# Kernel optimization log

Measured on AMD Instinct MI355X. Metric: run time of the kernel, lower is better.

Reference implementation:

```python
import jax, jax.numpy as jnp
import numpy as np

TOP_K = 2


def setup_inputs() -> dict:
    key = jax.random.key(0)
    k1, k2 = jax.random.split(key)
    x = jax.random.normal(k1, (4, 4096, 2048), dtype=jnp.float32)
    W = jax.random.normal(k2, (64, 2048), dtype=jnp.float32) * (1.0 / np.sqrt(2048))
    return {"x": x, "W": W}


def reference(x, W):
    B, S, D = x.shape
    E = W.shape[0]
    # logits: [B*S, E] via linear router (no bias)
    flat = x.reshape(-1, D)
    logits = jnp.einsum('td,ed->te', flat, W)
    probs = jax.nn.softmax(logits, axis=-1)
    # eval path: top-k indices
    _, top_k_indices = jax.lax.top_k(probs, TOP_K)          # [T, K]
    # scatter 1s -> mask; scatter gathered probs -> router_probs (== probs*mask)
    router_mask = jax.nn.one_hot(top_k_indices, E, dtype=probs.dtype).sum(axis=-2)  # [T, E]
    router_probs = probs * router_mask
    # normalize (top_k > 1: gradient flows through the sum)
    router_probs = router_probs / router_probs.sum(axis=-1, keepdims=True)
    return (router_mask.reshape(B, S, E),
            top_k_indices.reshape(B, S, TOP_K),
            router_probs.reshape(B, S, E),
            probs.reshape(B, S, E))
```

## Files before the change

### kernel.cpp

```cpp
#include <hip/hip_runtime.h>
#include <math.h>


#define D_DIM 2048
#define E_DIM 64

typedef __bf16 bf16x8 __attribute__((ext_vector_type(8)));
typedef unsigned short us8 __attribute__((ext_vector_type(8)));
typedef float f32x4 __attribute__((ext_vector_type(4)));

static __device__ __forceinline__ unsigned short f2bf(float f) {
    unsigned int u = __float_as_uint(f);
    u += 0x7fffu + ((u >> 16) & 1u);
    return (unsigned short)(u >> 16);
}
static __device__ __forceinline__ float bf2f(unsigned short h) {
    return __uint_as_float(((unsigned int)h) << 16);
}
static __device__ __forceinline__ void split4(const float4 v, ushort4* h, ushort4* l) {
    h->x = f2bf(v.x); l->x = f2bf(v.x - bf2f(h->x));
    h->y = f2bf(v.y); l->y = f2bf(v.y - bf2f(h->y));
    h->z = f2bf(v.z); l->z = f2bf(v.z - bf2f(h->z));
    h->w = f2bf(v.w); l->w = f2bf(v.w - bf2f(h->w));
}

static __device__ __forceinline__ void gld_lds16(const void* g, void* l) {
    __builtin_amdgcn_global_load_lds(
        (const __attribute__((address_space(1))) unsigned int*)g,
        (__attribute__((address_space(3))) unsigned int*)l,
        16, 0, 0);
}

__global__ __launch_bounds__(256, 1) void convert_w(
    const float4* __restrict__ W4, unsigned short* __restrict__ WH,
    unsigned short* __restrict__ WL)
{
    int i = blockIdx.x * 256 + threadIdx.x;
    float4 v = W4[i];
    ushort4 h, l;
    split4(v, &h, &l);
    *(ushort4*)&WH[i * 4] = h;
    *(ushort4*)&WL[i * 4] = l;
}

__global__ __launch_bounds__(256, 4) void router_fused(
    const float* __restrict__ x,
    const unsigned short* __restrict__ WHg, const unsigned short* __restrict__ WLg,
    float* __restrict__ mask_out, float* __restrict__ idx_out,
    float* __restrict__ rp_out, float* __restrict__ probs_out)
{
    __shared__ __align__(16) float          XF [2][16 * 64];
    __shared__ __align__(16) unsigned short WHs[2][64 * 64];
    __shared__ __align__(16) unsigned short WLs[2][64 * 64];

    const int tid  = threadIdx.x;
    const int lane = tid & 63;
    const int wv   = tid >> 6;
    const int quad = lane >> 4;
    const int l16  = lane & 15;

    const int t0  = blockIdx.x << 4;
    const int NCH = D_DIM >> 6;

    f32x4 acc = {0.f, 0.f, 0.f, 0.f};

    const int xrow = tid >> 4;
    const int xcg  = (tid & 15) ^ (xrow & 15);
    const int we   = wv * 8 + (lane >> 3);
    const int wo   = lane & 7;

    {
        gld_lds16(x + (size_t)(t0 + xrow) * D_DIM + xcg * 4,
                  &XF[0][(wv * 64) * 4]);
        #pragma unroll
        for (int i2 = 0; i2 < 2; ++i2) {
            int e  = i2 * 32 + we;
            int og = wo ^ (e & 7);
            gld_lds16(WHg + (size_t)e * D_DIM + og * 8,
                      &WHs[0][(i2 * 256 + wv * 64) * 8]);
            gld_lds16(WLg + (size_t)e * D_DIM + og * 8,
                      &WLs[0][(i2 * 256 + wv * 64) * 8]);
        }
    }
    __syncthreads();

    int buf = 0;
    for (int ch = 0; ch < NCH; ++ch) {
        if (ch + 1 < NCH) {
            const int kc = (ch + 1) << 6;
            const int nb = buf ^ 1;
            gld_lds16(x + (size_t)(t0 + xrow) * D_DIM + kc + xcg * 4,
                      &XF[nb][(wv * 64) * 4]);
            #pragma unroll
            for (int i2 = 0; i2 < 2; ++i2) {
                int e  = i2 * 32 + we;
                int og = wo ^ (e & 7);
                gld_lds16(WHg + (size_t)e * D_DIM + kc + og * 8,
                          &WHs[nb][(i2 * 256 + wv * 64) * 8]);
                gld_lds16(WLg + (size_t)e * D_DIM + kc + og * 8,
                          &WLs[nb][(i2 * 256 + wv * 64) * 8]);
            }
        }

        #pragma unroll
        for (int ks = 0; ks < 2; ++ks) {
            const int tr = l16;
            const int c0 = ks * 8 + quad * 2;
            float4 xa = *(const float4*)&XF[buf][(tr * 16 + ( c0      ^ (tr & 15))) * 4];
            float4 xb = *(const float4*)&XF[buf][(tr * 16 + ((c0 + 1) ^ (tr & 15))) * 4];
            ushort4 h0, l0, h1, l1;
            split4(xa, &h0, &l0);
            split4(xb, &h1, &l1);
            union { us8 u; bf16x8 b; } ua, ul;
            ua.u = (us8){h0.x, h0.y, h0.z, h0.w, h1.x, h1.y, h1.z, h1.w};
            ul.u = (us8){l0.x, l0.y, l0.z, l0.w, l1.x, l1.y, l1.z, l1.w};

            const int e = wv * 16 + l16;
            const int o = ks * 4 + quad;
            const int s = e * 8 + (o ^ (e & 7));
            bf16x8 bh = *(const bf16x8*)&WHs[buf][s * 8];
            bf16x8 bl = *(const bf16x8*)&WLs[buf][s * 8];
            acc = __builtin_amdgcn_mfma_f32_16x16x32_bf16(ua.b, bh, acc, 0, 0, 0);
            acc = __builtin_amdgcn_mfma_f32_16x16x32_bf16(ul.b, bh, acc, 0, 0, 0);
            acc = __builtin_amdgcn_mfma_f32_16x16x32_bf16(ua.b, bl, acc, 0, 0, 0);
        }
        __syncthreads();
        buf ^= 1;
    }

    float* L = &XF[0][0];
    #pragma unroll
    for (int r = 0; r < 4; ++r)
        L[(quad * 4 + r) * 64 + wv * 16 + l16] = acc[r];
    __syncthreads();

    for (int i = 0; i < 4; ++i) {
        const int tl = wv * 4 + i;
        const int t  = t0 + tl;
        const float v = L[tl * 64 + lane];

        float bv = v; int bi = lane;
        #pragma unroll
        for (int off = 1; off < 64; off <<= 1) {
            float ov = __shfl_xor(bv, off, 64);
            int   oi = __shfl_xor(bi, off, 64);
            bool take = (ov > bv) || (ov == bv && oi < bi);
            bv = take ? ov : bv;
            bi = take ? oi : bi;
        }
        const float m = bv; const int i1 = bi;

        const float p = __expf(v - m);
        float s = p;
        #pragma unroll
        for (int off = 1; off < 64; off <<= 1) s += __shfl_xor(s, off, 64);
        const float prob = p / s;

        const float v2 = (lane == i1) ? -INFINITY : v;
        float cv = v2; int ci = lane;
        #pragma unroll
        for (int off = 1; off < 64; off <<= 1) {
            float ov = __shfl_xor(cv, off, 64);
            int   oi = __shfl_xor(ci, off, 64);
            bool take = (ov > cv) || (ov == cv && oi < ci);
            cv = take ? ov : cv;
            ci = take ? oi : ci;
        }
        const int i2 = ci;

        const float pd = __shfl(prob, i1, 64) + __shfl(prob, i2, 64);
        const bool top = (lane == i1) || (lane == i2);

        const size_t base = (size_t)t * 64 + lane;
        mask_out[base]  = top ? 1.f : 0.f;
        rp_out[base]    = top ? prob / pd : 0.f;
        probs_out[base] = prob;
        if (lane == 0) {
            idx_out[(size_t)t * 2]     = (float)i1;
            idx_out[(size_t)t * 2 + 1] = (float)i2;
        }
    }
}

extern "C" void kernel_launch(void* const* d_in, const int* in_sizes, int n_in,
                              void* d_out, int out_size, void* d_ws, size_t ws_size,
                              hipStream_t stream) {
    const float* x = (const float*)d_in[0];
    const float* W = (const float*)d_in[1];
    float* out = (float*)d_out;

    const int T  = in_sizes[0] / D_DIM;
    const int WN = in_sizes[1];

    unsigned short* WH = (unsigned short*)d_ws;
    unsigned short* WL = WH + WN;

    float* mask_out  = out;
    float* idx_out   = out + (size_t)T * E_DIM;
    float* rp_out    = idx_out + (size_t)T * 2;
    float* probs_out = rp_out + (size_t)T * E_DIM;

    convert_w<<<dim3(WN / 1024), dim3(256), 0, stream>>>((const float4*)W, WH, WL);
    router_fused<<<dim3(T / 16), dim3(256), 0, stream>>>(
        x, WH, WL, mask_out, idx_out, rp_out, probs_out);
}
```

Baseline: 221.3 us.

## Split x into bf16 hi/lo once per element via register prefetch

```diff
diff --git a/kernel.cpp b/kernel.cpp
--- a/kernel.cpp
+++ b/kernel.cpp
@@ -4,6 +4,7 @@
 
 #define D_DIM 2048
 #define E_DIM 64
+#define NCH   (D_DIM >> 6)
 
 typedef __bf16 bf16x8 __attribute__((ext_vector_type(8)));
 typedef unsigned short us8 __attribute__((ext_vector_type(8)));
@@ -49,7 +50,8 @@
     float* __restrict__ mask_out, float* __restrict__ idx_out,
     float* __restrict__ rp_out, float* __restrict__ probs_out)
 {
-    __shared__ __align__(16) float          XF [2][16 * 64];
+    __shared__ __align__(16) unsigned short XH [2][16 * 64];
+    __shared__ __align__(16) unsigned short XL [2][16 * 64];
     __shared__ __align__(16) unsigned short WHs[2][64 * 64];
     __shared__ __align__(16) unsigned short WLs[2][64 * 64];
 
@@ -59,38 +61,50 @@
     const int quad = lane >> 4;
     const int l16  = lane & 15;
 
-    const int t0  = blockIdx.x << 4;
-    const int NCH = D_DIM >> 6;
+    const int t0 = blockIdx.x << 4;
 
     f32x4 acc = {0.f, 0.f, 0.f, 0.f};
 
-    const int xrow = tid >> 4;
-    const int xcg  = (tid & 15) ^ (xrow & 15);
-    const int we   = wv * 8 + (lane >> 3);
-    const int wo   = lane & 7;
-
-    {
-        gld_lds16(x + (size_t)(t0 + xrow) * D_DIM + xcg * 4,
-                  &XF[0][(wv * 64) * 4]);
-        #pragma unroll
-        for (int i2 = 0; i2 < 2; ++i2) {
-            int e  = i2 * 32 + we;
-            int og = wo ^ (e & 7);
-            gld_lds16(WHg + (size_t)e * D_DIM + og * 8,
-                      &WHs[0][(i2 * 256 + wv * 64) * 8]);
-            gld_lds16(WLg + (size_t)e * D_DIM + og * 8,
-                      &WLs[0][(i2 * 256 + wv * 64) * 8]);
-        }
+    const int we = wv * 8 + (lane >> 3);
+    const int wo = lane & 7;
+
+    const float* xg = x + (size_t)(t0 + l16) * D_DIM + wv * 16 + quad * 4;
+
+    const int g   = wv * 4 + quad;
+    const int cwb = l16 * 128 + (((g >> 1) ^ (l16 & 7)) << 4) + (g & 1) * 8;
+
+    float4 xc = *(const float4*)(xg);
+    #pragma unroll
+    for (int i2 = 0; i2 < 2; ++i2) {
+        int e  = i2 * 32 + we;
+        int og = wo ^ (e & 7);
+        gld_lds16(WHg + (size_t)e * D_DIM + og * 8, &WHs[0][(i2 * 256 + wv * 64) * 8]);
+        gld_lds16(WLg + (size_t)e * D_DIM + og * 8, &WLs[0][(i2 * 256 + wv * 64) * 8]);
     }
-    __syncthreads();
-
-    int buf = 0;
+
     for (int ch = 0; ch < NCH; ++ch) {
+        const int b = ch & 1;
+
+        float4 xn;
+        if (ch + 1 < NCH) xn = *(const float4*)(xg + (ch + 1) * 64);
+
+        {
+            ushort4 h, l;
+            split4(xc, &h, &l);
+            *(ushort4*)((char*)&XH[b][0] + cwb) = h;
+            *(ushort4*)((char*)&XL[b][0] + cwb) = l;
+        }
+
+        if (ch + 1 < NCH) asm volatile("s_waitcnt vmcnt(1)" ::: "memory");
+        else              asm volatile("s_waitcnt vmcnt(0)" ::: "memory");
+        asm volatile("s_waitcnt lgkmcnt(0)" ::: "memory");
+        __builtin_amdgcn_sched_barrier(0);
+        __builtin_amdgcn_s_barrier();
+        __builtin_amdgcn_sched_barrier(0);
+
         if (ch + 1 < NCH) {
             const int kc = (ch + 1) << 6;
-            const int nb = buf ^ 1;
-            gld_lds16(x + (size_t)(t0 + xrow) * D_DIM + kc + xcg * 4,
-                      &XF[nb][(wv * 64) * 4]);
+            const int nb = b ^ 1;
             #pragma unroll
             for (int i2 = 0; i2 < 2; ++i2) {
                 int e  = i2 * 32 + we;
@@ -104,31 +118,25 @@
 
         #pragma unroll
         for (int ks = 0; ks < 2; ++ks) {
-            const int tr = l16;
-            const int c0 = ks * 8 + quad * 2;
-            float4 xa = *(const float4*)&XF[buf][(tr * 16 + ( c0      ^ (tr & 15))) * 4];
-            float4 xb = *(const float4*)&XF[buf][(tr * 16 + ((c0 + 1) ^ (tr & 15))) * 4];
-            ushort4 h0, l0, h1, l1;
-            split4(xa, &h0, &l0);
-            split4(xb, &h1, &l1);
-            union { us8 u; bf16x8 b; } ua, ul;
-            ua.u = (us8){h0.x, h0.y, h0.z, h0.w, h1.x, h1.y, h1.z, h1.w};
-            ul.u = (us8){l0.x, l0.y, l0.z, l0.w, l1.x, l1.y, l1.z, l1.w};
+            const int sr = ks * 4 + quad;
+            const int ab = l16 * 128 + ((sr ^ (l16 & 7)) << 4);
+            bf16x8 ah = *(const bf16x8*)((const char*)&XH[b][0] + ab);
+            bf16x8 al = *(const bf16x8*)((const char*)&XL[b][0] + ab);
 
             const int e = wv * 16 + l16;
             const int o = ks * 4 + quad;
             const int s = e * 8 + (o ^ (e & 7));
-            bf16x8 bh = *(const bf16x8*)&WHs[buf][s * 8];
-            bf16x8 bl = *(const bf16x8*)&WLs[buf][s * 8];
-            acc = __builtin_amdgcn_mfma_f32_16x16x32_bf16(ua.b, bh, acc, 0, 0, 0);
-            acc = __builtin_amdgcn_mfma_f32_16x16x32_bf16(ul.b, bh, acc, 0, 0, 0);
-            acc = __builtin_amdgcn_mfma_f32_16x16x32_bf16(ua.b, bl, acc, 0, 0, 0);
-        }
-        __syncthreads();
-        buf ^= 1;
+            bf16x8 bh = *(const bf16x8*)&WHs[b][s * 8];
+            bf16x8 bl = *(const bf16x8*)&WLs[b][s * 8];
+            acc = __builtin_amdgcn_mfma_f32_16x16x32_bf16(ah, bh, acc, 0, 0, 0);
+            acc = __builtin_amdgcn_mfma_f32_16x16x32_bf16(al, bh, acc, 0, 0, 0);
+            acc = __builtin_amdgcn_mfma_f32_16x16x32_bf16(ah, bl, acc, 0, 0, 0);
+        }
+
+        if (ch + 1 < NCH) xc = xn;
     }
 
-    float* L = &XF[0][0];
+    float* L = (float*)&WHs[0][0];
     #pragma unroll
     for (int r = 0; r < 4; ++r)
         L[(quad * 4 + r) * 64 + wv * 16 + l16] = acc[r];
```

Result: no change. 218.3 us (-1.3%).

## Split K across waves with direct global loads instead of LDS double buffering

Applied to the files above, without the earlier changes.

```diff
diff --git a/kernel.cpp b/kernel.cpp
--- a/kernel.cpp
+++ b/kernel.cpp
@@ -24,13 +24,6 @@
     h->w = f2bf(v.w); l->w = f2bf(v.w - bf2f(h->w));
 }
 
-static __device__ __forceinline__ void gld_lds16(const void* g, void* l) {
-    __builtin_amdgcn_global_load_lds(
-        (const __attribute__((address_space(1))) unsigned int*)g,
-        (__attribute__((address_space(3))) unsigned int*)l,
-        16, 0, 0);
-}
-
 __global__ __launch_bounds__(256, 1) void convert_w(
     const float4* __restrict__ W4, unsigned short* __restrict__ WH,
     unsigned short* __restrict__ WL)
@@ -49,95 +42,59 @@
     float* __restrict__ mask_out, float* __restrict__ idx_out,
     float* __restrict__ rp_out, float* __restrict__ probs_out)
 {
-    __shared__ __align__(16) float          XF [2][16 * 64];
-    __shared__ __align__(16) unsigned short WHs[2][64 * 64];
-    __shared__ __align__(16) unsigned short WLs[2][64 * 64];
+    __shared__ __align__(16) float Lp[4][16 * 64];
 
     const int tid  = threadIdx.x;
     const int lane = tid & 63;
     const int wv   = tid >> 6;
     const int quad = lane >> 4;
     const int l16  = lane & 15;
+    const int t0   = blockIdx.x << 4;
 
-    const int t0  = blockIdx.x << 4;
-    const int NCH = D_DIM >> 6;
+    const int k0 = wv << 9;
 
-    f32x4 acc = {0.f, 0.f, 0.f, 0.f};
+    const float*          xp  = x   + (size_t)(t0 + l16) * D_DIM + k0 + quad * 8;
+    const unsigned short* whp = WHg + (size_t)l16 * D_DIM + k0 + quad * 8;
+    const unsigned short* wlp = WLg + (size_t)l16 * D_DIM + k0 + quad * 8;
 
-    const int xrow = tid >> 4;
-    const int xcg  = (tid & 15) ^ (xrow & 15);
-    const int we   = wv * 8 + (lane >> 3);
-    const int wo   = lane & 7;
+    f32x4 acc[4];
+    #pragma unroll
+    for (int n = 0; n < 4; ++n) { f32x4 z = {0.f, 0.f, 0.f, 0.f}; acc[n] = z; }
 
-    {
-        gld_lds16(x + (size_t)(t0 + xrow) * D_DIM + xcg * 4,
-                  &XF[0][(wv * 64) * 4]);
+    #pragma unroll 2
+    for (int j = 0; j < 16; ++j) {
+        const int o = j << 5;
+        float4 xa = *(const float4*)(xp + o);
+        float4 xb = *(const float4*)(xp + o + 4);
+        ushort4 h0, l0, h1, l1;
+        split4(xa, &h0, &l0);
+        split4(xb, &h1, &l1);
+        union { us8 u; bf16x8 b; } ua, ul;
+        ua.u = (us8){h0.x, h0.y, h0.z, h0.w, h1.x, h1.y, h1.z, h1.w};
+        ul.u = (us8){l0.x, l0.y, l0.z, l0.w, l1.x, l1.y, l1.z, l1.w};
+
         #pragma unroll
-        for (int i2 = 0; i2 < 2; ++i2) {
-            int e  = i2 * 32 + we;
-            int og = wo ^ (e & 7);
-            gld_lds16(WHg + (size_t)e * D_DIM + og * 8,
-                      &WHs[0][(i2 * 256 + wv * 64) * 8]);
-            gld_lds16(WLg + (size_t)e * D_DIM + og * 8,
-                      &WLs[0][(i2 * 256 + wv * 64) * 8]);
+        for (int n = 0; n < 4; ++n) {
+            bf16x8 bh = *(const bf16x8*)(whp + n * 16 * D_DIM + o);
+            bf16x8 bl = *(const bf16x8*)(wlp + n * 16 * D_DIM + o);
+            acc[n] = __builtin_amdgcn_mfma_f32_16x16x32_bf16(ua.b, bh, acc[n], 0, 0, 0);
+            acc[n] = __builtin_amdgcn_mfma_f32_16x16x32_bf16(ul.b, bh, acc[n], 0, 0, 0);
+            acc[n] = __builtin_amdgcn_mfma_f32_16x16x32_bf16(ua.b, bl, acc[n], 0, 0, 0);
         }
     }
-    __syncthreads();
 
-    int buf = 0;
-    for (int ch = 0; ch < NCH; ++ch) {
-        if (ch + 1 < NCH) {
-            const int kc = (ch + 1) << 6;
-            const int nb = buf ^ 1;
-            gld_lds16(x + (size_t)(t0 + xrow) * D_DIM + kc + xcg * 4,
-                      &XF[nb][(wv * 64) * 4]);
-            #pragma unroll
-            for (int i2 = 0; i2 < 2; ++i2) {
-                int e  = i2 * 32 + we;
-                int og = wo ^ (e & 7);
-                gld_lds16(WHg + (size_t)e * D_DIM + kc + og * 8,
-                          &WHs[nb][(i2 * 256 + wv * 64) * 8]);
-                gld_lds16(WLg + (size_t)e * D_DIM + kc + og * 8,
-                          &WLs[nb][(i2 * 256 + wv * 64) * 8]);
-            }
-        }
-
+    #pragma unroll
+    for (int n = 0; n < 4; ++n)
         #pragma unroll
-        for (int ks = 0; ks < 2; ++ks) {
-            const int tr = l16;
-            const int c0 = ks * 8 + quad * 2;
-            float4 xa = *(const float4*)&XF[buf][(tr * 16 + ( c0      ^ (tr & 15))) * 4];
-            float4 xb = *(const float4*)&XF[buf][(tr * 16 + ((c0 + 1) ^ (tr & 15))) * 4];
-            ushort4 h0, l0, h1, l1;
-            split4(xa, &h0, &l0);
-            split4(xb, &h1, &l1);
-            union { us8 u; bf16x8 b; } ua, ul;
-            ua.u = (us8){h0.x, h0.y, h0.z, h0.w, h1.x, h1.y, h1.z, h1.w};
-            ul.u = (us8){l0.x, l0.y, l0.z, l0.w, l1.x, l1.y, l1.z, l1.w};
-
-            const int e = wv * 16 + l16;
-            const int o = ks * 4 + quad;
-            const int s = e * 8 + (o ^ (e & 7));
-            bf16x8 bh = *(const bf16x8*)&WHs[buf][s * 8];
-            bf16x8 bl = *(const bf16x8*)&WLs[buf][s * 8];
-            acc = __builtin_amdgcn_mfma_f32_16x16x32_bf16(ua.b, bh, acc, 0, 0, 0);
-            acc = __builtin_amdgcn_mfma_f32_16x16x32_bf16(ul.b, bh, acc, 0, 0, 0);
-            acc = __builtin_amdgcn_mfma_f32_16x16x32_bf16(ua.b, bl, acc, 0, 0, 0);
-        }
-        __syncthreads();
-        buf ^= 1;
-    }
-
-    float* L = &XF[0][0];
-    #pragma unroll
-    for (int r = 0; r < 4; ++r)
-        L[(quad * 4 + r) * 64 + wv * 16 + l16] = acc[r];
+        for (int r = 0; r < 4; ++r)
+            Lp[wv][(quad * 4 + r) * 64 + n * 16 + l16] = acc[n][r];
     __syncthreads();
 
     for (int i = 0; i < 4; ++i) {
         const int tl = wv * 4 + i;
         const int t  = t0 + tl;
-        const float v = L[tl * 64 + lane];
+        const float v = Lp[0][tl * 64 + lane] + Lp[1][tl * 64 + lane]
+                      + Lp[2][tl * 64 + lane] + Lp[3][tl * 64 + lane];
 
         float bv = v; int bi = lane;
         #pragma unroll
```

After: 248.5 us. 1.12x slower.
